# Kernel optimization log

Hardware: AMD Instinct MI355X
Metric: run time of the kernel (lower is better)

## Reference

```python
import jax, jax.numpy as jnp
import numpy as np

B, KV, HID = 64, 2048, 4096
H, KVH, D = 32, 8, 128
G = H // KVH  # GQA group size = 4
THETA = 10000.0
SCALE = D ** -0.5


def setup_inputs() -> dict:
    key = jax.random.key(0)
    ks = jax.random.split(key, 7)
    hidden_states = jax.random.normal(ks[0], (B, HID), jnp.float32)
    k_cache = jax.random.normal(ks[1], (B, KV, KVH, D), jnp.float32)
    v_cache = jax.random.normal(ks[2], (B, KV, KVH, D), jnp.float32)
    # decode step: every sequence has KV cached tokens; new token at position KV
    positions = jnp.full((B,), KV, dtype=jnp.int32)
    Wqkv = jax.random.normal(ks[3], (HID, (H + 2 * KVH) * D), jnp.float32) * 0.02
    bqkv = jax.random.normal(ks[4], ((H + 2 * KVH) * D,), jnp.float32) * 0.02
    Wo = jax.random.normal(ks[5], (HID, HID), jnp.float32) * 0.02
    bo = jax.random.normal(ks[6], (HID,), jnp.float32) * 0.02
    return {"hidden_states": hidden_states, "k_cache": k_cache, "v_cache": v_cache,
            "positions": positions, "Wqkv": Wqkv, "bqkv": bqkv, "Wo": Wo, "bo": bo}


def _rope(x, pos):
    # x: [B, n_heads, D], pos: [B] int; neox-style (rotate halves)
    half = D // 2
    inv_freq = 1.0 / (THETA ** (jnp.arange(half, dtype=jnp.float32) * 2.0 / D))
    ang = pos[:, None].astype(jnp.float32) * inv_freq[None, :]        # [B, half]
    cos = jnp.cos(ang)[:, None, :].astype(x.dtype)                    # [B, 1, half]
    sin = jnp.sin(ang)[:, None, :].astype(x.dtype)
    x1, x2 = jnp.split(x, 2, axis=-1)
    return jnp.concatenate([x1 * cos - x2 * sin, x2 * cos + x1 * sin], axis=-1)


def reference(hidden_states, k_cache, v_cache, positions, Wqkv, bqkv, Wo, bo):
    qkv = hidden_states @ Wqkv + bqkv                                 # [B, (H+2KVH)*D]
    q, k_new, v_new = jnp.split(qkv, [H * D, (H + KVH) * D], axis=-1)
    q = q.reshape(B, H, D)
    k_new = k_new.reshape(B, KVH, D)
    v_new = v_new.reshape(B, KVH, D)

    q = _rope(q, positions)
    k_new = _rope(k_new, positions)

    keys = jnp.concatenate([k_cache, k_new[:, None]], axis=1)         # [B, KV+1, KVH, D]
    vals = jnp.concatenate([v_cache, v_new[:, None]], axis=1)

    qg = q.reshape(B, KVH, G, D)                                      # group Q heads per KV head
    scores = jnp.einsum('bkgd,bskd->bkgs', qg, keys) * SCALE          # [B, KVH, G, KV+1]
    probs = jax.nn.softmax(scores, axis=-1)
    attn = jnp.einsum('bkgs,bskd->bkgd', probs, vals)                 # [B, KVH, G, D]
    attn = attn.reshape(B, H * D)
    return attn @ Wo + bo                                             # [B, HID]
```

## Files before the change

kernel.cpp:

```cpp
#include <hip/hip_runtime.h>
#include <math.h>

#define BB 64
#define KVLEN 2048
#define HID 4096
#define NH 32
#define NKVH 8
#define DH 128
#define GQ 4
#define QKV_N ((NH + 2 * NKVH) * DH)

__global__ __launch_bounds__(256) void bias_init(float4* __restrict__ dst,
                                                 const float4* __restrict__ bias,
                                                 int ncols4, int total4) {
  int i = blockIdx.x * 256 + threadIdx.x;
  if (i < total4) dst[i] = bias[i % ncols4];
}

__global__ __launch_bounds__(256) void gemm_skinny(const float* __restrict__ A,
                                                   const float* __restrict__ W,
                                                   float* __restrict__ out,
                                                   int N, int K, int kchunk) {
  int lane = threadIdx.x & 63;
  int wave = __builtin_amdgcn_readfirstlane((int)(threadIdx.x >> 6));
  int n0 = blockIdx.x * 32 + wave * 8;
  int k0 = blockIdx.y * kchunk;
  const float* Arow = A + (size_t)lane * K + k0;
  const float* Wp = W + (size_t)k0 * N + n0;
  float acc[8] = {0.f, 0.f, 0.f, 0.f, 0.f, 0.f, 0.f, 0.f};
  for (int k = 0; k < kchunk; k += 8) {
    float4 a4a = *(const float4*)(Arow + k);
    float4 a4b = *(const float4*)(Arow + k + 4);
    float av[8] = {a4a.x, a4a.y, a4a.z, a4a.w, a4b.x, a4b.y, a4b.z, a4b.w};
    const float* w0 = Wp + (size_t)k * N;
#pragma unroll
    for (int kk = 0; kk < 8; ++kk) {
      const float* wr = w0 + (size_t)kk * N;
#pragma unroll
      for (int j = 0; j < 8; ++j)
        acc[j] = fmaf(av[kk], wr[j], acc[j]);
    }
  }
  float* op = out + (size_t)lane * N + n0;
#pragma unroll
  for (int j = 0; j < 8; ++j) atomicAdd(op + j, acc[j]);
}

__global__ __launch_bounds__(256) void rope_kernel(float* __restrict__ qkv,
                                                   const int* __restrict__ positions) {
  int idx = blockIdx.x * 256 + threadIdx.x;
  int d = idx & 63;
  int hb = idx >> 6;
  int head = hb % (NH + NKVH);
  int b = hb / (NH + NKVH);
  float* base = qkv + (size_t)b * QKV_N + (size_t)head * DH;
  double inv_freq = exp2(-(double)d * (13.287712379549449 / 64.0));
  double ang = (double)positions[b] * inv_freq;
  double sd, cd;
  sincos(ang, &sd, &cd);
  float c = (float)cd, s = (float)sd;
  float x1 = base[d], x2 = base[d + 64];
  float scale = (head < NH) ? 0.08838834764831845f : 1.0f;
  base[d] = (x1 * c - x2 * s) * scale;
  base[d + 64] = (x2 * c + x1 * s) * scale;
}

__global__ __launch_bounds__(256) void attn_kernel(const float* __restrict__ kc,
                                                   const float* __restrict__ vc,
                                                   const float* __restrict__ qkv,
                                                   float* __restrict__ attn) {
  int b = blockIdx.x >> 3;
  int kvh = blockIdx.x & 7;
  int tid = threadIdx.x;
  int lane = tid & 63;
  int wave = tid >> 6;

  __shared__ float q_s[4][DH];
  __shared__ float p_s[(KVLEN + 1) * 4];
  __shared__ float red[4][4];
  __shared__ float4 comb[128];

  const float* qb = qkv + (size_t)b * QKV_N + (size_t)(kvh * GQ) * DH;
  for (int i = tid; i < 4 * DH; i += 256) q_s[i >> 7][i & 127] = qb[i];
  __syncthreads();

  const float* Kb = kc + ((size_t)b * KVLEN * NKVH + kvh) * DH;
  float sc[8][4];
#pragma unroll
  for (int i = 0; i < 8; ++i) {
    int s = i * 256 + tid;
    const float4* kr = (const float4*)(Kb + (size_t)s * (NKVH * DH));
    float a0 = 0.f, a1 = 0.f, a2 = 0.f, a3 = 0.f;
#pragma unroll 8
    for (int d4 = 0; d4 < 32; ++d4) {
      float4 k4 = kr[d4];
      float4 q0 = *(const float4*)&q_s[0][d4 * 4];
      float4 q1 = *(const float4*)&q_s[1][d4 * 4];
      float4 q2 = *(const float4*)&q_s[2][d4 * 4];
      float4 q3 = *(const float4*)&q_s[3][d4 * 4];
      a0 = fmaf(k4.x, q0.x, fmaf(k4.y, q0.y, fmaf(k4.z, q0.z, fmaf(k4.w, q0.w, a0))));
      a1 = fmaf(k4.x, q1.x, fmaf(k4.y, q1.y, fmaf(k4.z, q1.z, fmaf(k4.w, q1.w, a1))));
      a2 = fmaf(k4.x, q2.x, fmaf(k4.y, q2.y, fmaf(k4.z, q2.z, fmaf(k4.w, q2.w, a2))));
      a3 = fmaf(k4.x, q3.x, fmaf(k4.y, q3.y, fmaf(k4.z, q3.z, fmaf(k4.w, q3.w, a3))));
    }
    sc[i][0] = a0; sc[i][1] = a1; sc[i][2] = a2; sc[i][3] = a3;
  }

  if (wave == 0) {
    const float* kn = qkv + (size_t)b * QKV_N + NH * DH + (size_t)kvh * DH;
    float k1v = kn[lane], k2v = kn[lane + 64];
    float pn[4];
#pragma unroll
    for (int h = 0; h < 4; ++h)
      pn[h] = k1v * q_s[h][lane] + k2v * q_s[h][lane + 64];
#pragma unroll
    for (int off = 32; off > 0; off >>= 1) {
#pragma unroll
      for (int h = 0; h < 4; ++h) pn[h] += __shfl_down(pn[h], off);
    }
    if (lane == 0) {
#pragma unroll
      for (int h = 0; h < 4; ++h) p_s[KVLEN * 4 + h] = pn[h];
    }
  }
  __syncthreads();

  float mxl[4];
#pragma unroll
  for (int h = 0; h < 4; ++h) mxl[h] = p_s[KVLEN * 4 + h];
#pragma unroll
  for (int i = 0; i < 8; ++i)
#pragma unroll
    for (int h = 0; h < 4; ++h) mxl[h] = fmaxf(mxl[h], sc[i][h]);
#pragma unroll
  for (int off = 32; off > 0; off >>= 1) {
#pragma unroll
    for (int h = 0; h < 4; ++h) mxl[h] = fmaxf(mxl[h], __shfl_xor(mxl[h], off));
  }
  if (lane == 0) {
#pragma unroll
    for (int h = 0; h < 4; ++h) red[wave][h] = mxl[h];
  }
  __syncthreads();
  float mx[4];
#pragma unroll
  for (int h = 0; h < 4; ++h)
    mx[h] = fmaxf(fmaxf(red[0][h], red[1][h]), fmaxf(red[2][h], red[3][h]));
  __syncthreads();

  float ls[4] = {0.f, 0.f, 0.f, 0.f};
#pragma unroll
  for (int i = 0; i < 8; ++i) {
    int s = i * 256 + tid;
#pragma unroll
    for (int h = 0; h < 4; ++h) {
      float e = __expf(sc[i][h] - mx[h]);
      p_s[s * 4 + h] = e;
      ls[h] += e;
    }
  }
  if (tid < 4) {
    float e = __expf(p_s[KVLEN * 4 + tid] - mx[tid]);
    p_s[KVLEN * 4 + tid] = e;
    ls[tid] += e;
  }
#pragma unroll
  for (int off = 32; off > 0; off >>= 1) {
#pragma unroll
    for (int h = 0; h < 4; ++h) ls[h] += __shfl_xor(ls[h], off);
  }
  if (lane == 0) {
#pragma unroll
    for (int h = 0; h < 4; ++h) red[wave][h] = ls[h];
  }
  __syncthreads();
  float inv[4];
#pragma unroll
  for (int h = 0; h < 4; ++h)
    inv[h] = 1.0f / (red[0][h] + red[1][h] + red[2][h] + red[3][h]);

  int half = tid >> 7;
  int r = tid & 127;
  int h = r >> 5;
  int d4 = r & 31;
  const float4* Vb = (const float4*)(vc + ((size_t)b * KVLEN * NKVH + kvh) * DH);
  float4 acc = {0.f, 0.f, 0.f, 0.f};
  int s0 = half * 1024;
  int s1 = s0 + 1024;
#pragma unroll 4
  for (int s = s0; s < s1; ++s) {
    float4 v4 = Vb[(size_t)s * (NKVH * DH / 4) + d4];
    float p = p_s[s * 4 + h];
    acc.x = fmaf(p, v4.x, acc.x);
    acc.y = fmaf(p, v4.y, acc.y);
    acc.z = fmaf(p, v4.z, acc.z);
    acc.w = fmaf(p, v4.w, acc.w);
  }
  if (half) {
    const float* vn = qkv + (size_t)b * QKV_N + (NH + NKVH) * DH + (size_t)kvh * DH;
    float4 v4 = *(const float4*)(vn + d4 * 4);
    float p = p_s[KVLEN * 4 + h];
    acc.x = fmaf(p, v4.x, acc.x);
    acc.y = fmaf(p, v4.y, acc.y);
    acc.z = fmaf(p, v4.z, acc.z);
    acc.w = fmaf(p, v4.w, acc.w);
    comb[r] = acc;
  }
  __syncthreads();
  if (!half) {
    float4 o = comb[r];
    float iv = inv[h];
    o.x = (o.x + acc.x) * iv;
    o.y = (o.y + acc.y) * iv;
    o.z = (o.z + acc.z) * iv;
    o.w = (o.w + acc.w) * iv;
    ((float4*)(attn + (size_t)b * HID + (size_t)kvh * (GQ * DH)))[r] = o;
  }
}

extern "C" void kernel_launch(void* const* d_in, const int* in_sizes, int n_in,
                              void* d_out, int out_size, void* d_ws, size_t ws_size,
                              hipStream_t stream) {
  (void)in_sizes; (void)n_in; (void)out_size; (void)ws_size;
  const float* h    = (const float*)d_in[0];
  const float* kc   = (const float*)d_in[1];
  const float* vc   = (const float*)d_in[2];
  const int*   pos  = (const int*)d_in[3];
  const float* Wqkv = (const float*)d_in[4];
  const float* bqkv = (const float*)d_in[5];
  const float* Wo   = (const float*)d_in[6];
  const float* bo   = (const float*)d_in[7];
  float* out = (float*)d_out;

  float* qkv  = (float*)d_ws;
  float* attn = qkv + (size_t)BB * QKV_N;

  bias_init<<<(BB * QKV_N / 4) / 256, 256, 0, stream>>>(
      (float4*)qkv, (const float4*)bqkv, QKV_N / 4, BB * QKV_N / 4);

  dim3 g1(QKV_N / 32, 4);
  gemm_skinny<<<g1, 256, 0, stream>>>(h, Wqkv, qkv, QKV_N, HID, HID / 4);

  rope_kernel<<<(BB * (NH + NKVH) * 64) / 256, 256, 0, stream>>>(qkv, pos);

  attn_kernel<<<BB * NKVH, 256, 0, stream>>>(kc, vc, qkv, attn);

  bias_init<<<(BB * HID / 4) / 256, 256, 0, stream>>>(
      (float4*)out, (const float4*)bo, HID / 4, BB * HID / 4);

  dim3 g2(HID / 32, 4);
  gemm_skinny<<<g2, 256, 0, stream>>>(attn, Wo, out, HID, HID, HID / 4);
}
```

Measured before the change: 1.466 ms.

## Transpose activations, split-K GEMM with partial buffers, widen attention blocks

Replaces the skinny GEMM with a version that reads a transposed activation matrix, so each lane owns one output column and W is read coalesced. Atomics are replaced by a 16-way split-K into partial buffers followed by a reduction kernel that also adds the bias. The attention kernel moves to 512 threads with four key streams per thread and a four-way split over V. It now writes its output transposed so the output GEMM can consume it directly. The cost is a large workspace for the partial sums and extra traffic to write and reduce them.

```diff
diff --git a/kernel.cpp b/kernel.cpp
--- a/kernel.cpp
+++ b/kernel.cpp
@@ -9,41 +9,65 @@
 #define DH 128
 #define GQ 4
 #define QKV_N ((NH + 2 * NKVH) * DH)
-
-__global__ __launch_bounds__(256) void bias_init(float4* __restrict__ dst,
-                                                 const float4* __restrict__ bias,
-                                                 int ncols4, int total4) {
-  int i = blockIdx.x * 256 + threadIdx.x;
-  if (i < total4) dst[i] = bias[i % ncols4];
-}
-
-__global__ __launch_bounds__(256) void gemm_skinny(const float* __restrict__ A,
-                                                   const float* __restrict__ W,
-                                                   float* __restrict__ out,
-                                                   int N, int K, int kchunk) {
+#define KSPLIT 16
+
+__global__ __launch_bounds__(256) void transpose64(const float* __restrict__ src,
+                                                   float* __restrict__ dst, int K) {
+  __shared__ float t[64][65];
+  int lane = threadIdx.x & 63;
+  int w = threadIdx.x >> 6;
+  int c0 = blockIdx.x * 64;
+#pragma unroll
+  for (int i = 0; i < 16; ++i) {
+    int r = w * 16 + i;
+    t[r][lane] = src[(size_t)r * K + c0 + lane];
+  }
+  __syncthreads();
+#pragma unroll
+  for (int i = 0; i < 16; ++i) {
+    int c = w * 16 + i;
+    dst[(size_t)(c0 + c) * 64 + lane] = t[lane][c];
+  }
+}
+
+__global__ __launch_bounds__(256) void gemm_skinny_t(const float* __restrict__ At,
+                                                     const float* __restrict__ W,
+                                                     float* __restrict__ part,
+                                                     int N, int kchunk) {
   int lane = threadIdx.x & 63;
   int wave = __builtin_amdgcn_readfirstlane((int)(threadIdx.x >> 6));
-  int n0 = blockIdx.x * 32 + wave * 8;
+  int r0 = wave * 16;
+  int n = blockIdx.x * 64 + lane;
   int k0 = blockIdx.y * kchunk;
-  const float* Arow = A + (size_t)lane * K + k0;
-  const float* Wp = W + (size_t)k0 * N + n0;
-  float acc[8] = {0.f, 0.f, 0.f, 0.f, 0.f, 0.f, 0.f, 0.f};
-  for (int k = 0; k < kchunk; k += 8) {
-    float4 a4a = *(const float4*)(Arow + k);
-    float4 a4b = *(const float4*)(Arow + k + 4);
-    float av[8] = {a4a.x, a4a.y, a4a.z, a4a.w, a4b.x, a4b.y, a4b.z, a4b.w};
-    const float* w0 = Wp + (size_t)k * N;
-#pragma unroll
-    for (int kk = 0; kk < 8; ++kk) {
-      const float* wr = w0 + (size_t)kk * N;
-#pragma unroll
-      for (int j = 0; j < 8; ++j)
-        acc[j] = fmaf(av[kk], wr[j], acc[j]);
-    }
-  }
-  float* op = out + (size_t)lane * N + n0;
-#pragma unroll
-  for (int j = 0; j < 8; ++j) atomicAdd(op + j, acc[j]);
+  const float* Ap = At + (size_t)k0 * 64 + r0;
+  const float* Wp = W + (size_t)k0 * N + n;
+  float acc[16];
+#pragma unroll
+  for (int j = 0; j < 16; ++j) acc[j] = 0.f;
+#pragma unroll 4
+  for (int k = 0; k < kchunk; ++k) {
+    float wv = Wp[(size_t)k * N];
+    const float* a = Ap + (size_t)k * 64;
+#pragma unroll
+    for (int j = 0; j < 16; ++j) acc[j] = fmaf(a[j], wv, acc[j]);
+  }
+  float* op = part + ((size_t)blockIdx.y * 64 + r0) * N + n;
+#pragma unroll
+  for (int j = 0; j < 16; ++j) op[(size_t)j * N] = acc[j];
+}
+
+__global__ __launch_bounds__(256) void reduce_add(const float4* __restrict__ part,
+                                                  const float4* __restrict__ bias,
+                                                  float4* __restrict__ out,
+                                                  int n4, int total4, int nch) {
+  int i = blockIdx.x * 256 + threadIdx.x;
+  if (i >= total4) return;
+  float4 a = bias[i % n4];
+  for (int c = 0; c < nch; ++c) {
+    float4 p = part[(size_t)c * total4 + i];
+    a.x += p.x; a.y += p.y; a.z += p.z; a.w += p.w;
+  }
+  out[i] = a;
 }
 
 __global__ __launch_bounds__(256) void rope_kernel(float* __restrict__ qkv,
@@ -65,10 +89,16 @@
   base[d + 64] = (x2 * c + x1 * s) * scale;
 }
 
-__global__ __launch_bounds__(256) void attn_kernel(const float* __restrict__ kc,
-                                                   const float* __restrict__ vc,
-                                                   const float* __restrict__ qkv,
-                                                   float* __restrict__ attn) {
+#define DOT4(accrow, kv)                                                                  \
+  accrow[0] = fmaf(kv.x, q0.x, fmaf(kv.y, q0.y, fmaf(kv.z, q0.z, fmaf(kv.w, q0.w, accrow[0])))); \
+  accrow[1] = fmaf(kv.x, q1.x, fmaf(kv.y, q1.y, fmaf(kv.z, q1.z, fmaf(kv.w, q1.w, accrow[1])))); \
+  accrow[2] = fmaf(kv.x, q2.x, fmaf(kv.y, q2.y, fmaf(kv.z, q2.z, fmaf(kv.w, q2.w, accrow[2])))); \
+  accrow[3] = fmaf(kv.x, q3.x, fmaf(kv.y, q3.y, fmaf(kv.z, q3.z, fmaf(kv.w, q3.w, accrow[3]))));
+
+__global__ __launch_bounds__(512, 4) void attn_kernel(const float* __restrict__ kcache,
+                                                      const float* __restrict__ vcache,
+                                                      const float* __restrict__ qkv,
+                                                      float* __restrict__ attnT) {
   int b = blockIdx.x >> 3;
   int kvh = blockIdx.x & 7;
   int tid = threadIdx.x;
@@ -76,34 +106,38 @@
   int wave = tid >> 6;
 
   __shared__ float q_s[4][DH];
-  __shared__ float p_s[(KVLEN + 1) * 4];
-  __shared__ float red[4][4];
-  __shared__ float4 comb[128];
+  __shared__ float p_s[KVLEN * 4 + 4];
+  __shared__ float red[8][4];
+  __shared__ float4 comb[3][128];
 
   const float* qb = qkv + (size_t)b * QKV_N + (size_t)(kvh * GQ) * DH;
-  for (int i = tid; i < 4 * DH; i += 256) q_s[i >> 7][i & 127] = qb[i];
-  __syncthreads();
-
-  const float* Kb = kc + ((size_t)b * KVLEN * NKVH + kvh) * DH;
-  float sc[8][4];
-#pragma unroll
-  for (int i = 0; i < 8; ++i) {
-    int s = i * 256 + tid;
-    const float4* kr = (const float4*)(Kb + (size_t)s * (NKVH * DH));
-    float a0 = 0.f, a1 = 0.f, a2 = 0.f, a3 = 0.f;
-#pragma unroll 8
-    for (int d4 = 0; d4 < 32; ++d4) {
-      float4 k4 = kr[d4];
-      float4 q0 = *(const float4*)&q_s[0][d4 * 4];
-      float4 q1 = *(const float4*)&q_s[1][d4 * 4];
-      float4 q2 = *(const float4*)&q_s[2][d4 * 4];
-      float4 q3 = *(const float4*)&q_s[3][d4 * 4];
-      a0 = fmaf(k4.x, q0.x, fmaf(k4.y, q0.y, fmaf(k4.z, q0.z, fmaf(k4.w, q0.w, a0))));
-      a1 = fmaf(k4.x, q1.x, fmaf(k4.y, q1.y, fmaf(k4.z, q1.z, fmaf(k4.w, q1.w, a1))));
-      a2 = fmaf(k4.x, q2.x, fmaf(k4.y, q2.y, fmaf(k4.z, q2.z, fmaf(k4.w, q2.w, a2))));
-      a3 = fmaf(k4.x, q3.x, fmaf(k4.y, q3.y, fmaf(k4.z, q3.z, fmaf(k4.w, q3.w, a3))));
-    }
-    sc[i][0] = a0; sc[i][1] = a1; sc[i][2] = a2; sc[i][3] = a3;
+  q_s[tid >> 7][tid & 127] = qb[tid];
+  __syncthreads();
+
+  const float* Kb = kcache + ((size_t)b * KVLEN * NKVH + kvh) * DH;
+  float sc[4][4];
+#pragma unroll
+  for (int i = 0; i < 4; ++i)
+#pragma unroll
+    for (int hh = 0; hh < 4; ++hh) sc[i][hh] = 0.f;
+  const float4* kr0 = (const float4*)(Kb + (size_t)(tid) * (NKVH * DH));
+  const float4* kr1 = (const float4*)(Kb + (size_t)(tid + 512) * (NKVH * DH));
+  const float4* kr2 = (const float4*)(Kb + (size_t)(tid + 1024) * (NKVH * DH));
+  const float4* kr3 = (const float4*)(Kb + (size_t)(tid + 1536) * (NKVH * DH));
+#pragma unroll 4
+  for (int d4 = 0; d4 < 32; ++d4) {
+    float4 q0 = *(const float4*)&q_s[0][d4 * 4];
+    float4 q1 = *(const float4*)&q_s[1][d4 * 4];
+    float4 q2 = *(const float4*)&q_s[2][d4 * 4];
+    float4 q3 = *(const float4*)&q_s[3][d4 * 4];
+    float4 t0 = kr0[d4];
+    float4 t1 = kr1[d4];
+    float4 t2 = kr2[d4];
+    float4 t3 = kr3[d4];
+    DOT4(sc[0], t0)
+    DOT4(sc[1], t1)
+    DOT4(sc[2], t2)
+    DOT4(sc[3], t3)
   }
 
   if (wave == 0) {
@@ -129,7 +163,7 @@
 #pragma unroll
   for (int h = 0; h < 4; ++h) mxl[h] = p_s[KVLEN * 4 + h];
 #pragma unroll
-  for (int i = 0; i < 8; ++i)
+  for (int i = 0; i < 4; ++i)
 #pragma unroll
     for (int h = 0; h < 4; ++h) mxl[h] = fmaxf(mxl[h], sc[i][h]);
 #pragma unroll
@@ -144,14 +178,18 @@
   __syncthreads();
   float mx[4];
 #pragma unroll
-  for (int h = 0; h < 4; ++h)
-    mx[h] = fmaxf(fmaxf(red[0][h], red[1][h]), fmaxf(red[2][h], red[3][h]));
+  for (int h = 0; h < 4; ++h) {
+    float m = red[0][h];
+#pragma unroll
+    for (int w = 1; w < 8; ++w) m = fmaxf(m, red[w][h]);
+    mx[h] = m;
+  }
   __syncthreads();
 
   float ls[4] = {0.f, 0.f, 0.f, 0.f};
 #pragma unroll
-  for (int i = 0; i < 8; ++i) {
-    int s = i * 256 + tid;
+  for (int i = 0; i < 4; ++i) {
+    int s = i * 512 + tid;
 #pragma unroll
     for (int h = 0; h < 4; ++h) {
       float e = __expf(sc[i][h] - mx[h]);
@@ -176,18 +214,22 @@
   __syncthreads();
   float inv[4];
 #pragma unroll
-  for (int h = 0; h < 4; ++h)
-    inv[h] = 1.0f / (red[0][h] + red[1][h] + red[2][h] + red[3][h]);
-
-  int half = tid >> 7;
+  for (int h = 0; h < 4; ++h) {
+    float t = 0.f;
+#pragma unroll
+    for (int w = 0; w < 8; ++w) t += red[w][h];
+    inv[h] = 1.0f / t;
+  }
+
+  int quarter = tid >> 7;
   int r = tid & 127;
   int h = r >> 5;
   int d4 = r & 31;
-  const float4* Vb = (const float4*)(vc + ((size_t)b * KVLEN * NKVH + kvh) * DH);
+  const float4* Vb = (const float4*)(vcache + ((size_t)b * KVLEN * NKVH + kvh) * DH);
   float4 acc = {0.f, 0.f, 0.f, 0.f};
-  int s0 = half * 1024;
-  int s1 = s0 + 1024;
-#pragma unroll 4
+  int s0 = quarter * 512;
+  int s1 = s0 + 512;
+#pragma unroll 8
   for (int s = s0; s < s1; ++s) {
     float4 v4 = Vb[(size_t)s * (NKVH * DH / 4) + d4];
     float p = p_s[s * 4 + h];
@@ -196,7 +238,7 @@
     acc.z = fmaf(p, v4.z, acc.z);
     acc.w = fmaf(p, v4.w, acc.w);
   }
-  if (half) {
+  if (quarter == 3) {
     const float* vn = qkv + (size_t)b * QKV_N + (NH + NKVH) * DH + (size_t)kvh * DH;
     float4 v4 = *(const float4*)(vn + d4 * 4);
     float p = p_s[KVLEN * 4 + h];
@@ -204,17 +246,21 @@
     acc.y = fmaf(p, v4.y, acc.y);
     acc.z = fmaf(p, v4.z, acc.z);
     acc.w = fmaf(p, v4.w, acc.w);
-    comb[r] = acc;
-  }
-  __syncthreads();
-  if (!half) {
-    float4 o = comb[r];
+  }
+  if (quarter > 0) comb[quarter - 1][r] = acc;
+  __syncthreads();
+  if (quarter == 0) {
+    float4 c0 = comb[0][r], c1 = comb[1][r], c2 = comb[2][r];
     float iv = inv[h];
-    o.x = (o.x + acc.x) * iv;
-    o.y = (o.y + acc.y) * iv;
-    o.z = (o.z + acc.z) * iv;
-    o.w = (o.w + acc.w) * iv;
-    ((float4*)(attn + (size_t)b * HID + (size_t)kvh * (GQ * DH)))[r] = o;
+    float ox = (acc.x + c0.x + c1.x + c2.x) * iv;
+    float oy = (acc.y + c0.y + c1.y + c2.y) * iv;
+    float oz = (acc.z + c0.z + c1.z + c2.z) * iv;
+    float ow = (acc.w + c0.w + c1.w + c2.w) * iv;
+    float* op = attnT + ((size_t)(kvh * 512 + r * 4)) * 64 + b;
+    op[0] = ox;
+    op[64] = oy;
+    op[128] = oz;
+    op[192] = ow;
   }
 }
 
@@ -232,22 +278,29 @@
   const float* bo   = (const float*)d_in[7];
   float* out = (float*)d_out;
 
-  float* qkv  = (float*)d_ws;
-  float* attn = qkv + (size_t)BB * QKV_N;
-
-  bias_init<<<(BB * QKV_N / 4) / 256, 256, 0, stream>>>(
-      (float4*)qkv, (const float4*)bqkv, QKV_N / 4, BB * QKV_N / 4);
-
-  dim3 g1(QKV_N / 32, 4);
-  gemm_skinny<<<g1, 256, 0, stream>>>(h, Wqkv, qkv, QKV_N, HID, HID / 4);
+  float* ht    = (float*)d_ws;
+  float* qkv   = ht + (size_t)HID * BB;
+  float* part1 = qkv + (size_t)BB * QKV_N;
+  float* attnT = part1 + (size_t)KSPLIT * BB * QKV_N;
+  float* part2 = attnT + (size_t)HID * BB;
+
+  transpose64<<<HID / 64, 256, 0, stream>>>(h, ht, HID);
+
+  dim3 g1(QKV_N / 64, KSPLIT);
+  gemm_skinny_t<<<g1, 256, 0, stream>>>(ht, Wqkv, part1, QKV_N, HID / KSPLIT);
+
+  reduce_add<<<(BB * QKV_N / 4) / 256, 256, 0, stream>>>(
+      (const float4*)part1, (const float4*)bqkv, (float4*)qkv,
+      QKV_N / 4, BB * QKV_N / 4, KSPLIT);
 
   rope_kernel<<<(BB * (NH + NKVH) * 64) / 256, 256, 0, stream>>>(qkv, pos);
 
-  attn_kernel<<<BB * NKVH, 256, 0, stream>>>(kc, vc, qkv, attn);
-
-  bias_init<<<(BB * HID / 4) / 256, 256, 0, stream>>>(
-      (float4*)out, (const float4*)bo, HID / 4, BB * HID / 4);
-
-  dim3 g2(HID / 32, 4);
-  gemm_skinny<<<g2, 256, 0, stream>>>(attn, Wo, out, HID, HID, HID / 4);
-}
+  attn_kernel<<<BB * NKVH, 512, 0, stream>>>(kc, vc, qkv, attnT);
+
+  dim3 g2(HID / 64, KSPLIT);
+  gemm_skinny_t<<<g2, 256, 0, stream>>>(attnT, Wo, part2, HID, HID / KSPLIT);
+
+  reduce_add<<<(BB * HID / 4) / 256, 256, 0, stream>>>(
+      (const float4*)part2, (const float4*)bo, (float4*)out,
+      HID / 4, BB * HID / 4, KSPLIT);
+}
```

Measured after the change: 1.408 ms. 3.9% less time.
